# Kernel tuning notes

Hardware: AMD Instinct MI355X
Metric: run time of the kernel (lower is better)

## Reference

```python
import jax, jax.numpy as jnp
import numpy as np

N, D, H = 2048, 128, 40


def setup_inputs() -> dict:
    key = jax.random.key(0)
    kx, kw, kv = jax.random.split(key, 3)
    X = jax.random.normal(kx, (N, D), dtype=jnp.float32)
    # nn.Parameter(torch.randn(D, D) / D) per head, stacked over H
    W = jax.random.normal(kw, (H, D, D), dtype=jnp.float32) / D
    V = jax.random.normal(kv, (H, D, D), dtype=jnp.float32) / D
    return {"X": X, "W": W, "V": V}


def reference(X, W, V):
    d = X.shape[1]
    # scores[h] = X @ W[h] @ X.T / sqrt(D)   -> [H, N, N]
    XW = jnp.einsum("nd,hde->hne", X, W)
    scores = jnp.einsum("hne,me->hnm", XW, X) / jnp.sqrt(jnp.asarray(d, X.dtype))
    # softmax over dim=1 of the 2D per-head score matrix == last axis here
    weights = jax.nn.softmax(scores, axis=-1) + 1e-8
    # A[h] = weights[h] @ X @ V[h]; output = sum over heads -> [N, D]
    XV = jnp.einsum("md,hde->hme", X, V)
    out = jnp.einsum("hnm,hme->ne", weights, XV)
    return out
```

## Files before the change

kernel.cpp:

```cpp
#include <hip/hip_runtime.h>
#include <hip/hip_bf16.h>
#include <stdint.h>

#define N 2048
#define D 128
#define H 40
#define NT 16

typedef __attribute__((ext_vector_type(8))) short short8;
typedef __attribute__((ext_vector_type(4))) float float4v;
typedef __attribute__((ext_vector_type(16))) float float16v;
typedef __attribute__((ext_vector_type(4))) _Float16 half4v;

static __device__ __forceinline__ unsigned short f32_to_bf16(float f) {
  unsigned int u = __builtin_bit_cast(unsigned int, f);
  unsigned int rounding = 0x7FFFu + ((u >> 16) & 1u);
  return (unsigned short)((u + rounding) >> 16);
}

static __device__ __forceinline__ unsigned int pk2(float lo, float hi) {
  return (unsigned int)f32_to_bf16(lo) | ((unsigned int)f32_to_bf16(hi) << 16);
}

static __device__ __forceinline__ unsigned int pk2f(float lo, float hi) {
  unsigned int a = __builtin_bit_cast(unsigned int, lo) + 0x8000u;
  unsigned int b = __builtin_bit_cast(unsigned int, hi) + 0x8000u;
  return __builtin_amdgcn_perm(b, a, 0x07060302u);
}

static __device__ __forceinline__ unsigned long long pack4(float x0, float x1,
                                                           float x2, float x3) {
  return (unsigned long long)pk2(x0, x1) | ((unsigned long long)pk2(x2, x3) << 32);
}

static __device__ __forceinline__ float fast_exp2(float x) {
#if __has_builtin(__builtin_amdgcn_exp2f)
  return __builtin_amdgcn_exp2f(x);
#else
  return __expf(0.69314718056f * x);
#endif
}

static __device__ __forceinline__ float bf2f(unsigned short u) {
  unsigned int x = ((unsigned int)u) << 16;
  return __builtin_bit_cast(float, x);
}

static __device__ __forceinline__ long long mk64(unsigned int lo, unsigned int hi) {
  return (long long)(((unsigned long long)hi << 32) | lo);
}

static __device__ __forceinline__ void load_lds16(const void* g, void* l) {
  __builtin_amdgcn_global_load_lds(
      (const __attribute__((address_space(1))) unsigned int*)g,
      (__attribute__((address_space(3))) unsigned int*)l, 16, 0, 0);
}

#define MFMA32(a, b, c) __builtin_amdgcn_mfma_f32_32x32x16_bf16((a), (b), (c), 0, 0, 0)
#define MFMA8(a, b, c) __builtin_amdgcn_mfma_f32_32x32x16_fp8_fp8((a), (b), (c), 0, 0, 0)

static __device__ __forceinline__ void regs_to_bfrags(const float16v c, int hh,
                                                      short8& f0, short8& f1) {
  unsigned int a0 = pk2f(c[0], c[1]),   a1 = pk2f(c[2], c[3]);
  unsigned int a2 = pk2f(c[4], c[5]),   a3 = pk2f(c[6], c[7]);
  unsigned int a4 = pk2f(c[8], c[9]),   a5 = pk2f(c[10], c[11]);
  unsigned int a6 = pk2f(c[12], c[13]), a7 = pk2f(c[14], c[15]);
  unsigned int x0 = __shfl_xor(hh ? a0 : a2, 32);
  unsigned int x1 = __shfl_xor(hh ? a1 : a3, 32);
  unsigned int x2 = __shfl_xor(hh ? a4 : a6, 32);
  unsigned int x3 = __shfl_xor(hh ? a5 : a7, 32);
  uint4 u0 = {hh ? x0 : a0, hh ? x1 : a1, hh ? a2 : x0, hh ? a3 : x1};
  uint4 u1 = {hh ? x2 : a4, hh ? x3 : a5, hh ? a6 : x2, hh ? a7 : x3};
  f0 = __builtin_bit_cast(short8, u0);
  f1 = __builtin_bit_cast(short8, u1);
}

static __device__ __forceinline__ void regs_to_f8frags(const float16v c, int hh,
                                                       long long& f0, long long& f1) {
  const float s = 64.0f;
  int v0 = __builtin_amdgcn_cvt_pk_fp8_f32(c[0] * s, c[1] * s, 0, false);
  v0 = __builtin_amdgcn_cvt_pk_fp8_f32(c[2] * s, c[3] * s, v0, true);
  int v1 = __builtin_amdgcn_cvt_pk_fp8_f32(c[4] * s, c[5] * s, 0, false);
  v1 = __builtin_amdgcn_cvt_pk_fp8_f32(c[6] * s, c[7] * s, v1, true);
  int v2 = __builtin_amdgcn_cvt_pk_fp8_f32(c[8] * s, c[9] * s, 0, false);
  v2 = __builtin_amdgcn_cvt_pk_fp8_f32(c[10] * s, c[11] * s, v2, true);
  int v3 = __builtin_amdgcn_cvt_pk_fp8_f32(c[12] * s, c[13] * s, 0, false);
  v3 = __builtin_amdgcn_cvt_pk_fp8_f32(c[14] * s, c[15] * s, v3, true);
  int t0 = __shfl_xor(hh ? v0 : v1, 32);
  int t1 = __shfl_xor(hh ? v2 : v3, 32);
  f0 = hh ? mk64((unsigned)t0, (unsigned)v1) : mk64((unsigned)v0, (unsigned)t0);
  f1 = hh ? mk64((unsigned)t1, (unsigned)v3) : mk64((unsigned)v2, (unsigned)t1);
}

static __device__ __forceinline__ void regs_to_pfrags(const float16v s, int hh,
                                                      float& lsum, short8& f0,
                                                      short8& f1) {
  float e[16];
  float acc = 0.0f;
#pragma unroll
  for (int i = 0; i < 16; i++) { e[i] = fast_exp2(s[i] * 0.015625f); acc += e[i]; }
  lsum += acc;
  unsigned int a0 = pk2f(e[0], e[1]),   a1 = pk2f(e[2], e[3]);
  unsigned int a2 = pk2f(e[4], e[5]),   a3 = pk2f(e[6], e[7]);
  unsigned int a4 = pk2f(e[8], e[9]),   a5 = pk2f(e[10], e[11]);
  unsigned int a6 = pk2f(e[12], e[13]), a7 = pk2f(e[14], e[15]);
  unsigned int x0 = __shfl_xor(hh ? a0 : a2, 32);
  unsigned int x1 = __shfl_xor(hh ? a1 : a3, 32);
  unsigned int x2 = __shfl_xor(hh ? a4 : a6, 32);
  unsigned int x3 = __shfl_xor(hh ? a5 : a7, 32);
  uint4 u0 = {hh ? x0 : a0, hh ? x1 : a1, hh ? a2 : x0, hh ? a3 : x1};
  uint4 u1 = {hh ? x2 : a4, hh ? x3 : a5, hh ? a6 : x2, hh ? a7 : x3};
  f0 = __builtin_bit_cast(short8, u0);
  f1 = __builtin_bit_cast(short8, u1);
}

static __device__ __forceinline__ void stage_64x256(const char* gbase, size_t stride,
                                                    char* lds, int wave, int lane) {
#pragma unroll
  for (int i = 0; i < 4; i++) {
    int r = wave * 16 + i * 4 + (lane >> 4);
    int us = (lane & 15) ^ (r & 15);
    load_lds16(gbase + (size_t)r * stride + us * 16, lds + (wave * 16 + i * 4) * 256);
  }
}
static __device__ __forceinline__ void stage_128x256(const char* gbase, size_t stride,
                                                     char* lds, int wave, int lane) {
#pragma unroll
  for (int i = 0; i < 8; i++) {
    int r = wave * 32 + i * 4 + (lane >> 4);
    int us = (lane & 15) ^ (r & 15);
    load_lds16(gbase + (size_t)r * stride + us * 16, lds + (wave * 32 + i * 4) * 256);
  }
}
static __device__ __forceinline__ void stage_128x128(const char* gbase, size_t stride,
                                                     int colOff, char* lds, int wave,
                                                     int lane) {
#pragma unroll
  for (int i = 0; i < 4; i++) {
    int m = wave * 16 + i * 4 + (lane >> 4);
    int u = (lane & 15) ^ (m & 15);
    int grow = 2 * m + (u >> 3);
    load_lds16(gbase + (size_t)grow * stride + colOff + (u & 7) * 16,
               lds + (wave * 16 + i * 4) * 256);
  }
}
static __device__ __forceinline__ void stage_k8(const char* gbase, char* lds,
                                                int wave, int lane) {
#pragma unroll
  for (int i = 0; i < 2; i++) {
    int m = wave * 8 + i * 4 + (lane >> 4);
    int u = (lane & 15) ^ (m & 15);
    int grow = 2 * m + (u >> 3);
    load_lds16(gbase + (size_t)grow * 128 + (u & 7) * 16,
               lds + (wave * 8 + i * 4) * 256);
  }
}
static __device__ __forceinline__ short8 read_macro(const char* lds, int row, int kunit) {
  int m = row >> 1;
  int u = ((row & 1) << 3) | kunit;
  return *(const short8*)(lds + m * 256 + ((u ^ (m & 15)) * 16));
}

__global__ __launch_bounds__(256)
void prep_kernel(const float* __restrict__ X, const float* __restrict__ W,
                 const float* __restrict__ V, unsigned short* __restrict__ Xb,
                 unsigned short* __restrict__ XbT, unsigned char* __restrict__ Xf8,
                 unsigned short* __restrict__ Wt, unsigned short* __restrict__ Vt) {
  const int tid = threadIdx.x;
  __shared__ __align__(16) unsigned short Lt[128 * 136];
  if (blockIdx.x < 16) {
    const int n0 = blockIdx.x * 128;
    for (int i = tid; i < 128 * 32; i += 256) {
      int row = i >> 5, c4 = (i & 31) * 4;
      float4v x = *(const float4v*)(X + (size_t)(n0 + row) * D + c4);
      unsigned long long p = pack4(x.x, x.y, x.z, x.w);
      *(unsigned long long*)(Lt + row * 136 + c4) = p;
      *(unsigned long long*)(Xb + (size_t)(n0 + row) * D + c4) = p;
    }
    __syncthreads();
    for (int i = tid; i < 128 * 16; i += 256) {
      int d = i >> 4, g = i & 15;
      short8 v;
#pragma unroll
      for (int j = 0; j < 8; j++) v[j] = (short)Lt[(g * 8 + j) * 136 + d];
      *(short8*)(XbT + (size_t)d * N + n0 + g * 8) = v;
    }
    for (int i = tid; i < 128 * 8; i += 256) {
      int row = i >> 3, c = i & 7, t = c >> 1, o8 = (c & 1) * 8;
      const unsigned short* lp = Lt + row * 136;
      int d0 = t * 32 + o8, d1 = t * 32 + 16 + o8;
      short8 xa = *(const short8*)(lp + d0);
      short8 xb = *(const short8*)(lp + d1);
      int w0 = __builtin_amdgcn_cvt_pk_fp8_f32(bf2f(xa[0]), bf2f(xa[1]), 0, false);
      w0 = __builtin_amdgcn_cvt_pk_fp8_f32(bf2f(xa[2]), bf2f(xa[3]), w0, true);
      int w1 = __builtin_amdgcn_cvt_pk_fp8_f32(bf2f(xa[4]), bf2f(xa[5]), 0, false);
      w1 = __builtin_amdgcn_cvt_pk_fp8_f32(bf2f(xa[6]), bf2f(xa[7]), w1, true);
      int w2 = __builtin_amdgcn_cvt_pk_fp8_f32(bf2f(xb[0]), bf2f(xb[1]), 0, false);
      w2 = __builtin_amdgcn_cvt_pk_fp8_f32(bf2f(xb[2]), bf2f(xb[3]), w2, true);
      int w3 = __builtin_amdgcn_cvt_pk_fp8_f32(bf2f(xb[4]), bf2f(xb[5]), 0, false);
      w3 = __builtin_amdgcn_cvt_pk_fp8_f32(bf2f(xb[6]), bf2f(xb[7]), w3, true);
      uint4 st = {(unsigned)w0, (unsigned)w1, (unsigned)w2, (unsigned)w3};
      *(uint4*)(Xf8 + (size_t)(n0 + row) * 128 + c * 16) = st;
    }
  } else {
    const int b = blockIdx.x - 16;
    const int mat = (b >= H) ? 1 : 0;
    const int h = mat ? b - H : b;
    const float* src = (mat ? V : W) + (size_t)h * D * D;
    unsigned short* dst = (mat ? Vt : Wt) + (size_t)h * D * D;
    const float scale = mat ? 1.0f : 0.1275174313f;
    for (int i = tid; i < 128 * 32; i += 256) {
      int d = i >> 5, e4 = (i & 31) * 4;
      float4v w = *(const float4v*)(src + d * D + e4);
      Lt[(e4 + 0) * 136 + d] = f32_to_bf16(w.x * scale);
      Lt[(e4 + 1) * 136 + d] = f32_to_bf16(w.y * scale);
      Lt[(e4 + 2) * 136 + d] = f32_to_bf16(w.z * scale);
      Lt[(e4 + 3) * 136 + d] = f32_to_bf16(w.w * scale);
    }
    __syncthreads();
    for (int i = tid; i < 128 * 16; i += 256) {
      int e = i >> 4, u = i & 15;
      *(uint4*)((char*)dst + (size_t)e * 256 + u * 16) =
          *(const uint4*)((const char*)Lt + (size_t)e * 272 + u * 16);
    }
  }
}

__global__ __launch_bounds__(256)
void qprep_kernel(const unsigned short* __restrict__ Xb,
                  const unsigned short* __restrict__ Wt,
                  unsigned char* __restrict__ Qf8g) {
  __shared__ __align__(16) char smem[32768];
  const int bx = blockIdx.x;
  const int h = bx >> 4;
  const int q0 = (bx & 15) << 7;
  const int tid = threadIdx.x;
  const int wave = tid >> 6, lane = tid & 63;
  const int l = lane & 31, hh = lane >> 5;

  stage_128x256((const char*)(Wt + (size_t)h * D * D), 256, smem, wave, lane);
  short8 xfr[8];
#pragma unroll
  for (int dk = 0; dk < 8; dk++)
    xfr[dk] = *(const short8*)((const char*)Xb +
              (size_t)(q0 + wave * 32 + l) * 256 + dk * 32 + hh * 16);
  __syncthreads();

  float16v qa[4];
#pragma unroll
  for (int et = 0; et < 4; et++) qa[et] = (float16v)0.0f;
#pragma unroll
  for (int et = 0; et < 4; et++) {
    const int r = et * 32 + l;
#pragma unroll
    for (int dk = 0; dk < 8; dk++) {
      short8 wa = *(const short8*)(smem + r * 256 + (((2 * dk + hh) ^ (r & 15)) * 16));
      qa[et] = MFMA32(wa, xfr[dk], qa[et]);
    }
  }
  char* base = (char*)Qf8g + ((size_t)bx * 4 + wave) * 4096;
#pragma unroll
  for (int et = 0; et < 4; et++) {
    long long f0, f1;
    regs_to_f8frags(qa[et], hh, f0, f1);
    uint4 st = {(unsigned)(unsigned long long)f0,
                (unsigned)((unsigned long long)f0 >> 32),
                (unsigned)(unsigned long long)f1,
                (unsigned)((unsigned long long)f1 >> 32)};
    *(uint4*)(base + et * 1024 + lane * 16) = st;
  }
}

__global__ __launch_bounds__(256)
void attn_kernel(const unsigned char* __restrict__ Qf8g,
                 const unsigned char* __restrict__ Xf8,
                 const unsigned short* __restrict__ XbT,
                 const unsigned short* __restrict__ Vt,
                 unsigned short* __restrict__ Opart, float* __restrict__ Lsum) {
  __shared__ __align__(16) char smem[32768];
  char* Xbuf = smem;
  char* KA = smem + 16384;
  char* KB = smem + 24576;
  const int bx = blockIdx.x;
  const int kh = bx & 1;
  const int qt = (bx >> 1) & 15;
  const int q0 = qt << 7;
  const int h = bx >> 5;
  const int tid = threadIdx.x;
  const int wave = tid >> 6, lane = tid & 63;
  const int l = lane & 31, hh = lane >> 5;

  const char* Xf8B = (const char*)Xf8;
  const char* XbTB = (const char*)XbT;
  const char* VtB = (const char*)(Vt + (size_t)h * D * D);
  const int kbase = kh * (N / 2);

  stage_k8(Xf8B + (size_t)kbase * 128, KA, wave, lane);
  long long qf8[8];
  {
    const char* qp = (const char*)Qf8g + (((size_t)h * 16 + qt) * 4 + wave) * 4096;
#pragma unroll
    for (int i = 0; i < 4; i++) {
      uint4 v = *(const uint4*)(qp + i * 1024 + lane * 16);
      qf8[2 * i] = mk64(v.x, v.y);
      qf8[2 * i + 1] = mk64(v.z, v.w);
    }
  }
  float16v Tacc[4];
#pragma unroll
  for (int dt = 0; dt < 4; dt++) Tacc[dt] = (float16v)0.0f;
  float lsum = 0.0f;
  __syncthreads();

  for (int kt = 0; kt < NT; kt++) {
    const char* curK = (kt & 1) ? KB : KA;
    char* altK = (kt & 1) ? KA : KB;
    const int k0 = kbase + kt * 64;
    stage_128x128(XbTB, 4096, k0 * 2, Xbuf, wave, lane);
    if (kt + 1 < NT)
      stage_k8(Xf8B + (size_t)(k0 + 64) * 128, altK, wave, lane);
    float16v s0 = (float16v)0.0f, s1 = (float16v)0.0f;
    {
      const int m0 = l >> 1, r0 = (l & 1) << 3;
      const int m1 = (32 + l) >> 1;
#pragma unroll
      for (int t = 0; t < 4; t++) {
        int u0 = (r0 | (t * 2 + hh)) ^ (m0 & 15);
        int u1 = (r0 | (t * 2 + hh)) ^ (m1 & 15);
        uint4 w0 = *(const uint4*)(curK + m0 * 256 + u0 * 16);
        uint4 w1 = *(const uint4*)(curK + m1 * 256 + u1 * 16);
        s0 = MFMA8(mk64(w0.x, w0.y), qf8[2 * t], s0);
        s1 = MFMA8(mk64(w1.x, w1.y), qf8[2 * t], s1);
        s0 = MFMA8(mk64(w0.z, w0.w), qf8[2 * t + 1], s0);
        s1 = MFMA8(mk64(w1.z, w1.w), qf8[2 * t + 1], s1);
      }
    }
    short8 pf0[2], pf1[2];
    regs_to_pfrags(s0, hh, lsum, pf0[0], pf0[1]);
    regs_to_pfrags(s1, hh, lsum, pf1[0], pf1[1]);
    __syncthreads();
#pragma unroll
    for (int kk = 0; kk < 2; kk++)
#pragma unroll
      for (int dt = 0; dt < 4; dt++) {
        short8 xt0 = read_macro(Xbuf, dt * 32 + l, kk * 2 + hh);
        Tacc[dt] = MFMA32(xt0, pf0[kk], Tacc[dt]);
        short8 xt1 = read_macro(Xbuf, dt * 32 + l, 4 + kk * 2 + hh);
        Tacc[dt] = MFMA32(xt1, pf1[kk], Tacc[dt]);
      }
    __syncthreads();
  }

  float tot = lsum + __shfl_xor(lsum, 32);
  if (hh == 0) Lsum[(size_t)(h * 2 + kh) * N + q0 + wave * 32 + l] = tot;

  stage_64x256(VtB, 256, KA, wave, lane);
  stage_64x256(VtB + 64 * 256, 256, Xbuf, wave, lane);
  short8 tb[8];
#pragma unroll
  for (int dt = 0; dt < 4; dt++)
    regs_to_bfrags(Tacc[dt], hh, tb[2 * dt], tb[2 * dt + 1]);
  __syncthreads();

  float16v oacc[4];
#pragma unroll
  for (int et = 0; et < 4; et++) oacc[et] = (float16v)0.0f;
#pragma unroll
  for (int et = 0; et < 2; et++) {
    const int r = et * 32 + l;
#pragma unroll
    for (int dk = 0; dk < 8; dk++) {
      short8 va = *(const short8*)(KA + r * 256 + (((2 * dk + hh) ^ (r & 15)) * 16));
      oacc[et] = MFMA32(va, tb[dk], oacc[et]);
    }
  }
#pragma unroll
  for (int et = 2; et < 4; et++) {
    const int r = (et - 2) * 32 + l;
#pragma unroll
    for (int dk = 0; dk < 8; dk++) {
      short8 va = *(const short8*)(Xbuf + r * 256 + (((2 * dk + hh) ^ (r & 15)) * 16));
      oacc[et] = MFMA32(va, tb[dk], oacc[et]);
    }
  }

  unsigned short* Oph = Opart + (size_t)(h * 2 + kh) * N * D;
#pragma unroll
  for (int pass = 0; pass < 2; pass++) {
    __syncthreads();
    const int qrow = wave * 32 + l;
#pragma unroll
    for (int etL = 0; etL < 2; etL++) {
      int et = pass * 2 + etL;
#pragma unroll
      for (int g = 0; g < 4; g++) {
        int unit = etL * 8 + 2 * g + hh;
        float4v v;
        v.x = oacc[et][4 * g + 0];
        v.y = oacc[et][4 * g + 1];
        v.z = oacc[et][4 * g + 2];
        v.w = oacc[et][4 * g + 3];
        *(float4v*)(smem + qrow * 256 + ((unit ^ (qrow & 15)) * 16)) = v;
      }
    }
    __syncthreads();
#pragma unroll
    for (int i = 0; i < 8; i++) {
      int idx = i * 256 + tid;
      int qr = idx >> 4, up = idx & 15, u = up ^ (qr & 15);
      float4v v = *(const float4v*)(smem + qr * 256 + up * 16);
      auto h0 = __builtin_amdgcn_cvt_pkrtz(v.x, v.y);
      auto h1 = __builtin_amdgcn_cvt_pkrtz(v.z, v.w);
      uint2 st = {__builtin_bit_cast(unsigned int, h0),
                  __builtin_bit_cast(unsigned int, h1)};
      *(uint2*)(Oph + (size_t)(q0 + qr) * D + pass * 64 + u * 4) = st;
    }
  }
}

__global__ __launch_bounds__(256)
void reduce_kernel(const unsigned short* __restrict__ Opart,
                   const float* __restrict__ Lsum, float* __restrict__ out) {
  int idx = blockIdx.x * 256 + threadIdx.x;
  int n = idx >> 5;
  const uint2* base = (const uint2*)Opart;
  float4v acc = (float4v)0.0f;
#pragma unroll 8
  for (int h = 0; h < H; h++) {
    float lt = Lsum[(size_t)(2 * h) * N + n] + Lsum[(size_t)(2 * h + 1) * N + n];
    float il = __builtin_amdgcn_rcpf(lt);
    uint2 a = base[(size_t)(2 * h) * (N * D / 4) + idx];
    uint2 b = base[(size_t)(2 * h + 1) * (N * D / 4) + idx];
    float4v fa = __builtin_convertvector(__builtin_bit_cast(half4v, a), float4v);
    float4v fb = __builtin_convertvector(__builtin_bit_cast(half4v, b), float4v);
    acc += (fa + fb) * il;
  }
  *(float4v*)(out + (size_t)idx * 4) = acc;
}

extern "C" void kernel_launch(void* const* d_in, const int* in_sizes, int n_in,
                              void* d_out, int out_size, void* d_ws, size_t ws_size,
                              hipStream_t stream) {
  const float* X = (const float*)d_in[0];
  const float* W = (const float*)d_in[1];
  const float* V = (const float*)d_in[2];
  float* out = (float*)d_out;

  unsigned short* Xb = (unsigned short*)d_ws;
  unsigned short* XbT = Xb + (size_t)N * D;
  unsigned short* Wt = XbT + (size_t)N * D;
  unsigned short* Vt = Wt + (size_t)H * D * D;
  unsigned char* Xf8 = (unsigned char*)(Vt + (size_t)H * D * D);
  unsigned char* Qf8g = Xf8 + (size_t)N * D;
  unsigned short* Opart = (unsigned short*)(Qf8g + (size_t)H * 16 * 4 * 4096);
  float* Lsum = (float*)(Opart + (size_t)H * 2 * N * D);

  prep_kernel<<<dim3(16 + 2 * H), 256, 0, stream>>>(X, W, V, Xb, XbT, Xf8, Wt, Vt);
  qprep_kernel<<<dim3(16 * H), 256, 0, stream>>>(Xb, Wt, Qf8g);
  attn_kernel<<<dim3(NT * 2 * H), 256, 0, stream>>>(Qf8g, Xf8, XbT, Vt, Opart, Lsum);
  reduce_kernel<<<dim3(N * D / 4 / 256), 256, 0, stream>>>(Opart, Lsum, out);
}
```

Measured before the change: 195.6 us.

## Fuse Q projection into prep kernel and widen reduce grid

Merges qprep into prep_kernel: each Q block converts its head's W slice (with the score scale) straight from fp32 into swizzled LDS and converts its X rows to bf16 in registers. This drops the intermediate Xb/Wt buffers and one kernel launch. The cost is that the W conversion is repeated by each of the 16 q-tiles of a head, and LDS use grows. The reduce kernel now has each thread handle 2 outputs instead of 4, doubling the thread count to raise parallelism.

```diff
diff --git a/kernel.cpp b/kernel.cpp
--- a/kernel.cpp
+++ b/kernel.cpp
@@ -8,9 +8,10 @@
 #define NT 16
 
 typedef __attribute__((ext_vector_type(8))) short short8;
+typedef __attribute__((ext_vector_type(2))) float float2v;
 typedef __attribute__((ext_vector_type(4))) float float4v;
 typedef __attribute__((ext_vector_type(16))) float float16v;
-typedef __attribute__((ext_vector_type(4))) _Float16 half4v;
+typedef __attribute__((ext_vector_type(2))) _Float16 half2v;
 
 static __device__ __forceinline__ unsigned short f32_to_bf16(float f) {
   unsigned int u = __builtin_bit_cast(unsigned int, f);
@@ -123,15 +124,6 @@
     load_lds16(gbase + (size_t)r * stride + us * 16, lds + (wave * 16 + i * 4) * 256);
   }
 }
-static __device__ __forceinline__ void stage_128x256(const char* gbase, size_t stride,
-                                                     char* lds, int wave, int lane) {
-#pragma unroll
-  for (int i = 0; i < 8; i++) {
-    int r = wave * 32 + i * 4 + (lane >> 4);
-    int us = (lane & 15) ^ (r & 15);
-    load_lds16(gbase + (size_t)r * stride + us * 16, lds + (wave * 32 + i * 4) * 256);
-  }
-}
 static __device__ __forceinline__ void stage_128x128(const char* gbase, size_t stride,
                                                      int colOff, char* lds, int wave,
                                                      int lane) {
@@ -163,19 +155,20 @@
 
 __global__ __launch_bounds__(256)
 void prep_kernel(const float* __restrict__ X, const float* __restrict__ W,
-                 const float* __restrict__ V, unsigned short* __restrict__ Xb,
-                 unsigned short* __restrict__ XbT, unsigned char* __restrict__ Xf8,
-                 unsigned short* __restrict__ Wt, unsigned short* __restrict__ Vt) {
+                 const float* __restrict__ V, unsigned short* __restrict__ XbT,
+                 unsigned char* __restrict__ Xf8, unsigned short* __restrict__ Vt,
+                 unsigned char* __restrict__ Qf8g) {
   const int tid = threadIdx.x;
-  __shared__ __align__(16) unsigned short Lt[128 * 136];
-  if (blockIdx.x < 16) {
-    const int n0 = blockIdx.x * 128;
+  const int bx = blockIdx.x;
+  __shared__ __align__(16) char smem[34816];
+  unsigned short* Lt = (unsigned short*)smem;
+
+  if (bx < 16) {
+    const int n0 = bx * 128;
     for (int i = tid; i < 128 * 32; i += 256) {
       int row = i >> 5, c4 = (i & 31) * 4;
       float4v x = *(const float4v*)(X + (size_t)(n0 + row) * D + c4);
-      unsigned long long p = pack4(x.x, x.y, x.z, x.w);
-      *(unsigned long long*)(Lt + row * 136 + c4) = p;
-      *(unsigned long long*)(Xb + (size_t)(n0 + row) * D + c4) = p;
+      *(unsigned long long*)(Lt + row * 136 + c4) = pack4(x.x, x.y, x.z, x.w);
     }
     __syncthreads();
     for (int i = tid; i < 128 * 16; i += 256) {
@@ -202,20 +195,17 @@
       uint4 st = {(unsigned)w0, (unsigned)w1, (unsigned)w2, (unsigned)w3};
       *(uint4*)(Xf8 + (size_t)(n0 + row) * 128 + c * 16) = st;
     }
-  } else {
-    const int b = blockIdx.x - 16;
-    const int mat = (b >= H) ? 1 : 0;
-    const int h = mat ? b - H : b;
-    const float* src = (mat ? V : W) + (size_t)h * D * D;
-    unsigned short* dst = (mat ? Vt : Wt) + (size_t)h * D * D;
-    const float scale = mat ? 1.0f : 0.1275174313f;
+  } else if (bx < 56) {
+    const int h = bx - 16;
+    const float* src = V + (size_t)h * D * D;
+    unsigned short* dst = Vt + (size_t)h * D * D;
     for (int i = tid; i < 128 * 32; i += 256) {
       int d = i >> 5, e4 = (i & 31) * 4;
       float4v w = *(const float4v*)(src + d * D + e4);
-      Lt[(e4 + 0) * 136 + d] = f32_to_bf16(w.x * scale);
-      Lt[(e4 + 1) * 136 + d] = f32_to_bf16(w.y * scale);
-      Lt[(e4 + 2) * 136 + d] = f32_to_bf16(w.z * scale);
-      Lt[(e4 + 3) * 136 + d] = f32_to_bf16(w.w * scale);
+      Lt[(e4 + 0) * 136 + d] = f32_to_bf16(w.x);
+      Lt[(e4 + 1) * 136 + d] = f32_to_bf16(w.y);
+      Lt[(e4 + 2) * 136 + d] = f32_to_bf16(w.z);
+      Lt[(e4 + 3) * 136 + d] = f32_to_bf16(w.w);
     }
     __syncthreads();
     for (int i = tid; i < 128 * 16; i += 256) {
@@ -223,51 +213,63 @@
       *(uint4*)((char*)dst + (size_t)e * 256 + u * 16) =
           *(const uint4*)((const char*)Lt + (size_t)e * 272 + u * 16);
     }
-  }
-}
-
-__global__ __launch_bounds__(256)
-void qprep_kernel(const unsigned short* __restrict__ Xb,
-                  const unsigned short* __restrict__ Wt,
-                  unsigned char* __restrict__ Qf8g) {
-  __shared__ __align__(16) char smem[32768];
-  const int bx = blockIdx.x;
-  const int h = bx >> 4;
-  const int q0 = (bx & 15) << 7;
-  const int tid = threadIdx.x;
-  const int wave = tid >> 6, lane = tid & 63;
-  const int l = lane & 31, hh = lane >> 5;
-
-  stage_128x256((const char*)(Wt + (size_t)h * D * D), 256, smem, wave, lane);
-  short8 xfr[8];
-#pragma unroll
-  for (int dk = 0; dk < 8; dk++)
-    xfr[dk] = *(const short8*)((const char*)Xb +
-              (size_t)(q0 + wave * 32 + l) * 256 + dk * 32 + hh * 16);
-  __syncthreads();
-
-  float16v qa[4];
-#pragma unroll
-  for (int et = 0; et < 4; et++) qa[et] = (float16v)0.0f;
-#pragma unroll
-  for (int et = 0; et < 4; et++) {
-    const int r = et * 32 + l;
+  } else {
+    const int qb = bx - 56;
+    const int h = qb >> 4;
+    const int q0 = (qb & 15) << 7;
+    const int wave = tid >> 6, lane = tid & 63;
+    const int l = lane & 31, hh = lane >> 5;
+    const float scale = 0.1275174313f;
+
+    const float* Wh = W + (size_t)h * D * D;
+    for (int i = tid; i < 128 * 32; i += 256) {
+      int d = i >> 5, e4 = (i & 31) * 4;
+      float4v w = *(const float4v*)(Wh + d * D + e4);
+      int ub = ((d >> 3) * 16);
+      int db = (d & 7) * 2;
+      *(unsigned short*)(smem + (e4 + 0) * 256 + (ub ^ (((e4 + 0) & 15) * 16)) + db) =
+          f32_to_bf16(w.x * scale);
+      *(unsigned short*)(smem + (e4 + 1) * 256 + (ub ^ (((e4 + 1) & 15) * 16)) + db) =
+          f32_to_bf16(w.y * scale);
+      *(unsigned short*)(smem + (e4 + 2) * 256 + (ub ^ (((e4 + 2) & 15) * 16)) + db) =
+          f32_to_bf16(w.z * scale);
+      *(unsigned short*)(smem + (e4 + 3) * 256 + (ub ^ (((e4 + 3) & 15) * 16)) + db) =
+          f32_to_bf16(w.w * scale);
+    }
+    short8 xfr[8];
+    const float* Xrow = X + (size_t)(q0 + wave * 32 + l) * D;
 #pragma unroll
     for (int dk = 0; dk < 8; dk++) {
-      short8 wa = *(const short8*)(smem + r * 256 + (((2 * dk + hh) ^ (r & 15)) * 16));
-      qa[et] = MFMA32(wa, xfr[dk], qa[et]);
-    }
-  }
-  char* base = (char*)Qf8g + ((size_t)bx * 4 + wave) * 4096;
-#pragma unroll
-  for (int et = 0; et < 4; et++) {
-    long long f0, f1;
-    regs_to_f8frags(qa[et], hh, f0, f1);
-    uint4 st = {(unsigned)(unsigned long long)f0,
-                (unsigned)((unsigned long long)f0 >> 32),
-                (unsigned)(unsigned long long)f1,
-                (unsigned)((unsigned long long)f1 >> 32)};
-    *(uint4*)(base + et * 1024 + lane * 16) = st;
+      float4v a = *(const float4v*)(Xrow + dk * 16 + hh * 8);
+      float4v b = *(const float4v*)(Xrow + dk * 16 + hh * 8 + 4);
+      uint4 u = {pk2(a.x, a.y), pk2(a.z, a.w), pk2(b.x, b.y), pk2(b.z, b.w)};
+      xfr[dk] = __builtin_bit_cast(short8, u);
+    }
+    __syncthreads();
+
+    float16v qa[4];
+#pragma unroll
+    for (int et = 0; et < 4; et++) qa[et] = (float16v)0.0f;
+#pragma unroll
+    for (int et = 0; et < 4; et++) {
+      const int r = et * 32 + l;
+#pragma unroll
+      for (int dk = 0; dk < 8; dk++) {
+        short8 wa = *(const short8*)(smem + r * 256 + (((2 * dk + hh) ^ (r & 15)) * 16));
+        qa[et] = MFMA32(wa, xfr[dk], qa[et]);
+      }
+    }
+    char* base = (char*)Qf8g + ((size_t)qb * 4 + wave) * 4096;
+#pragma unroll
+    for (int et = 0; et < 4; et++) {
+      long long f0, f1;
+      regs_to_f8frags(qa[et], hh, f0, f1);
+      uint4 st = {(unsigned)(unsigned long long)f0,
+                  (unsigned)((unsigned long long)f0 >> 32),
+                  (unsigned)(unsigned long long)f1,
+                  (unsigned)((unsigned long long)f1 >> 32)};
+      *(uint4*)(base + et * 1024 + lane * 16) = st;
+    }
   }
 }
 
@@ -422,20 +424,20 @@
 void reduce_kernel(const unsigned short* __restrict__ Opart,
                    const float* __restrict__ Lsum, float* __restrict__ out) {
   int idx = blockIdx.x * 256 + threadIdx.x;
-  int n = idx >> 5;
-  const uint2* base = (const uint2*)Opart;
-  float4v acc = (float4v)0.0f;
+  int n = idx >> 6;
+  const unsigned int* base = (const unsigned int*)Opart;
+  float2v acc = (float2v)0.0f;
 #pragma unroll 8
   for (int h = 0; h < H; h++) {
     float lt = Lsum[(size_t)(2 * h) * N + n] + Lsum[(size_t)(2 * h + 1) * N + n];
     float il = __builtin_amdgcn_rcpf(lt);
-    uint2 a = base[(size_t)(2 * h) * (N * D / 4) + idx];
-    uint2 b = base[(size_t)(2 * h + 1) * (N * D / 4) + idx];
-    float4v fa = __builtin_convertvector(__builtin_bit_cast(half4v, a), float4v);
-    float4v fb = __builtin_convertvector(__builtin_bit_cast(half4v, b), float4v);
+    unsigned int a = base[(size_t)(2 * h) * (N * D / 2) + idx];
+    unsigned int b = base[(size_t)(2 * h + 1) * (N * D / 2) + idx];
+    float2v fa = __builtin_convertvector(__builtin_bit_cast(half2v, a), float2v);
+    float2v fb = __builtin_convertvector(__builtin_bit_cast(half2v, b), float2v);
     acc += (fa + fb) * il;
   }
-  *(float4v*)(out + (size_t)idx * 4) = acc;
+  *(float2v*)(out + (size_t)idx * 2) = acc;
 }
 
 extern "C" void kernel_launch(void* const* d_in, const int* in_sizes, int n_in,
@@ -446,17 +448,14 @@
   const float* V = (const float*)d_in[2];
   float* out = (float*)d_out;
 
-  unsigned short* Xb = (unsigned short*)d_ws;
-  unsigned short* XbT = Xb + (size_t)N * D;
-  unsigned short* Wt = XbT + (size_t)N * D;
-  unsigned short* Vt = Wt + (size_t)H * D * D;
+  unsigned short* XbT = (unsigned short*)d_ws;
+  unsigned short* Vt = XbT + (size_t)N * D;
   unsigned char* Xf8 = (unsigned char*)(Vt + (size_t)H * D * D);
   unsigned char* Qf8g = Xf8 + (size_t)N * D;
   unsigned short* Opart = (unsigned short*)(Qf8g + (size_t)H * 16 * 4 * 4096);
   float* Lsum = (float*)(Opart + (size_t)H * 2 * N * D);
 
-  prep_kernel<<<dim3(16 + 2 * H), 256, 0, stream>>>(X, W, V, Xb, XbT, Xf8, Wt, Vt);
-  qprep_kernel<<<dim3(16 * H), 256, 0, stream>>>(Xb, Wt, Qf8g);
+  prep_kernel<<<dim3(56 + 16 * H), 256, 0, stream>>>(X, W, V, XbT, Xf8, Vt, Qf8g);
   attn_kernel<<<dim3(NT * 2 * H), 256, 0, stream>>>(Qf8g, Xf8, XbT, Vt, Opart, Lsum);
-  reduce_kernel<<<dim3(N * D / 4 / 256), 256, 0, stream>>>(Opart, Lsum, out);
-}
+  reduce_kernel<<<dim3(N * D / 2 / 256), 256, 0, stream>>>(Opart, Lsum, out);
+}
```

Result: faster. 191.5 us (-2.1%).
